# Kernel tuning notes

Measured on AMD Instinct MI355X. Metric: run time of the kernel, lower is better.

Reference implementation:

```python
import jax, jax.numpy as jnp
import numpy as np

B, S, D, V = 4, 512, 512, 32000
GAMMA = 0.5
EPS = 1e-12  # torch F.normalize clamp_min eps


def _l2norm(x, axis):
    n = jnp.sqrt(jnp.sum(x * x, axis=axis, keepdims=True))
    return x / jnp.maximum(n, EPS)


def setup_inputs() -> dict:
    key = jax.random.key(0)
    k1, k2, k3 = jax.random.split(key, 3)
    preds = jax.random.normal(k1, (B, D, S), dtype=jnp.float32)
    emb_weight = jax.random.normal(k2, (V, D), dtype=jnp.float32)
    target = jax.random.randint(k3, (B, S), 0, V, dtype=jnp.int64)
    return {"preds": preds, "emb_weight": emb_weight, "target": target, "pad_id": 0}


def reference(preds, emb_weight, target, pad_id):
    # preds: [B, D, S] -> [B, S, D], L2-normalized over D
    out_norm = _l2norm(jnp.transpose(preds, (0, 2, 1)), axis=2)
    voc_norm = _l2norm(emb_weight, axis=1)          # [V, D]
    tgt_emb = emb_weight[target]                     # [B, S, D] (raw lookup, not normalized)
    mask = target != pad_id                          # [B, S]

    cos_out_voc = jnp.einsum('bsd,vd->bsv', out_norm, voc_norm)  # [B, S, V]
    tgt_voc = jnp.einsum('bsd,vd->bsv', tgt_emb, voc_norm)       # [B, S, V]

    jmax = jnp.argmax(cos_out_voc - tgt_voc, axis=2)             # [B, S]
    cos_target = jnp.take_along_axis(cos_out_voc, target[..., None], axis=2)[..., 0]
    max_cos_voc = jnp.take_along_axis(cos_out_voc, jmax[..., None], axis=2)[..., 0]

    diff = jnp.maximum(GAMMA + max_cos_voc - cos_target, 0.0)    # [B, S]
    denom = jnp.sum(mask).astype(diff.dtype)
    return jnp.sum(jnp.where(mask, diff, 0.0)) / denom
```

## Files before the change

kernel.cpp:

```cpp
#include <hip/hip_runtime.h>
#include <math.h>


#define Bb 4
#define Ss 512
#define Dd 512
#define Vv 32000
#define ROWS (Bb * Ss)
#define NTILE_M (ROWS / 128)
#define NTILE_N (Vv / 128)

typedef __attribute__((ext_vector_type(8))) short bf16x8;
typedef __attribute__((ext_vector_type(4))) float f32x4;

__device__ __forceinline__ float waveReduceSum(float x) {
#pragma unroll
  for (int m = 32; m >= 1; m >>= 1) x += __shfl_xor(x, m, 64);
  return x;
}

__device__ __forceinline__ unsigned short f2bf(float f) {
  unsigned u = __float_as_uint(f);
  unsigned r = (u + 0x7FFFu + ((u >> 16) & 1u)) >> 16;
  return (unsigned short)r;
}

__device__ __forceinline__ unsigned long long packSC(float s, int c) {
  unsigned b = __float_as_uint(s);
  unsigned key = b ^ ((b & 0x80000000u) ? 0xFFFFFFFFu : 0x80000000u);
  return ((unsigned long long)key << 32) | (unsigned)(~c);
}

__device__ __forceinline__ void async_ld16(const void* g, void* l) {
  __builtin_amdgcn_global_load_lds((const __attribute__((address_space(1))) void*)g,
                                   (__attribute__((address_space(3))) void*)l, 16, 0, 0);
}

__global__ __launch_bounds__(256) void prep_rows(
    const float* __restrict__ preds, const float* __restrict__ emb,
    const int* __restrict__ target,
    float* __restrict__ o_rows, short* __restrict__ u_bf,
    float* __restrict__ cos_tgt) {
  int row = blockIdx.x;
  int b = row >> 9, s = row & (Ss - 1);
  int tid = threadIdx.x;
  int wave = tid >> 6, lane = tid & 63;
  const float* p = preds + (size_t)b * Dd * Ss + s;
  float x0 = p[(size_t)tid * Ss];
  float x1 = p[(size_t)(tid + 256) * Ss];
  __shared__ float red[12];
  float ss = waveReduceSum(x0 * x0 + x1 * x1);
  if (lane == 0) red[wave] = ss;
  __syncthreads();
  float inv = 1.0f / fmaxf(sqrtf(red[0] + red[1] + red[2] + red[3]), 1e-12f);
  float o0 = x0 * inv, o1 = x1 * inv;
  o_rows[(size_t)row * Dd + tid] = o0;
  o_rows[(size_t)row * Dd + tid + 256] = o1;
  int t = target[row];
  const float* et = emb + (size_t)t * Dd;
  float e0 = et[tid], e1 = et[tid + 256];
  u_bf[(size_t)row * Dd + tid] = (short)f2bf(o0 - e0);
  u_bf[(size_t)row * Dd + tid + 256] = (short)f2bf(o1 - e1);
  float ss2 = waveReduceSum(e0 * e0 + e1 * e1);
  float dt = waveReduceSum(o0 * e0 + o1 * e1);
  if (lane == 0) { red[4 + wave] = ss2; red[8 + wave] = dt; }
  __syncthreads();
  if (tid == 0) {
    float n2 = red[4] + red[5] + red[6] + red[7];
    float dd = red[8] + red[9] + red[10] + red[11];
    cos_tgt[row] = dd * (1.0f / fmaxf(sqrtf(n2), 1e-12f));
  }
}

__global__ __launch_bounds__(256) void voc_prep(const float* __restrict__ emb,
                                                short* __restrict__ ebf,
                                                float* __restrict__ inv_norm) {
  int v = blockIdx.x * 4 + (threadIdx.x >> 6);
  int lane = threadIdx.x & 63;
  const float* e = emb + (size_t)v * Dd;
  float4 x0 = *(const float4*)(e + lane * 8);
  float4 x1 = *(const float4*)(e + lane * 8 + 4);
  float ss = x0.x * x0.x + x0.y * x0.y + x0.z * x0.z + x0.w * x0.w +
             x1.x * x1.x + x1.y * x1.y + x1.z * x1.z + x1.w * x1.w;
  ss = waveReduceSum(ss);
  float inv = 1.0f / fmaxf(sqrtf(ss), 1e-12f);
  bf16x8 o;
  o[0] = (short)f2bf(x0.x * inv); o[1] = (short)f2bf(x0.y * inv);
  o[2] = (short)f2bf(x0.z * inv); o[3] = (short)f2bf(x0.w * inv);
  o[4] = (short)f2bf(x1.x * inv); o[5] = (short)f2bf(x1.y * inv);
  o[6] = (short)f2bf(x1.z * inv); o[7] = (short)f2bf(x1.w * inv);
  *(bf16x8*)(ebf + (size_t)v * Dd + lane * 8) = o;
  if (lane == 0) inv_norm[v] = inv;
}

__global__ __launch_bounds__(256) void gemm_argmax(
    const short* __restrict__ u_bf, const short* __restrict__ ebf,
    unsigned long long* __restrict__ part) {
  __shared__ short sA[128 * 32];
  __shared__ short sB[128 * 32];
  int tm = blockIdx.x, tn = blockIdx.y;
  int tid = threadIdx.x;
  int w = tid >> 6, lane = tid & 63;
  int wm = w >> 1, wn = w & 1;

  const short* gA = u_bf + ((size_t)(tm * 128 + w * 32 + (lane >> 2)) * Dd) + (lane & 3) * 8;
  const short* gB = ebf + ((size_t)(tn * 128 + w * 32 + (lane >> 2)) * Dd) + (lane & 3) * 8;
  short* lA = &sA[(w * 32) * 32];
  short* lB = &sB[(w * 32) * 32];

  const short* pa = &sA[(lane & 15) * 32 + (lane >> 4) * 8];
  const short* pb = &sB[(lane & 15) * 32 + (lane >> 4) * 8];

  f32x4 acc[4][4];
  f32x4 z = {0.f, 0.f, 0.f, 0.f};
#pragma unroll
  for (int mi = 0; mi < 4; ++mi)
#pragma unroll
    for (int ni = 0; ni < 4; ++ni) acc[mi][ni] = z;

  for (int kk = 0; kk < Dd / 32; ++kk) {
    __syncthreads();
    async_ld16(gA + kk * 32, lA);
    async_ld16(gA + 16 * Dd + kk * 32, lA + 16 * 32);
    async_ld16(gB + kk * 32, lB);
    async_ld16(gB + 16 * Dd + kk * 32, lB + 16 * 32);
    __syncthreads();
    bf16x8 af[4], bg[4];
#pragma unroll
    for (int mi = 0; mi < 4; ++mi)
      af[mi] = *(const bf16x8*)(pa + (wm * 64 + mi * 16) * 32);
#pragma unroll
    for (int ni = 0; ni < 4; ++ni)
      bg[ni] = *(const bf16x8*)(pb + (wn * 64 + ni * 16) * 32);
#pragma unroll
    for (int mi = 0; mi < 4; ++mi)
#pragma unroll
      for (int ni = 0; ni < 4; ++ni)
        acc[mi][ni] = __builtin_amdgcn_mfma_f32_16x16x32_bf16(af[mi], bg[ni], acc[mi][ni], 0, 0, 0);
  }

  float bs[4][4];
  int bc[4][4];
  int col0 = tn * 128 + wn * 64 + (lane & 15);
#pragma unroll
  for (int mi = 0; mi < 4; ++mi) {
#pragma unroll
    for (int j = 0; j < 4; ++j) { bs[mi][j] = acc[mi][0][j]; bc[mi][j] = col0; }
#pragma unroll
    for (int ni = 1; ni < 4; ++ni) {
      int c = col0 + ni * 16;
#pragma unroll
      for (int j = 0; j < 4; ++j) {
        float v = acc[mi][ni][j];
        if (v > bs[mi][j]) { bs[mi][j] = v; bc[mi][j] = c; }
      }
    }
  }
#pragma unroll
  for (int m = 1; m < 16; m <<= 1) {
#pragma unroll
    for (int mi = 0; mi < 4; ++mi)
#pragma unroll
      for (int j = 0; j < 4; ++j) {
        float os = __shfl_xor(bs[mi][j], m, 64);
        int oc = __shfl_xor(bc[mi][j], m, 64);
        if (os > bs[mi][j] || (os == bs[mi][j] && oc < bc[mi][j])) {
          bs[mi][j] = os;
          bc[mi][j] = oc;
        }
      }
  }
  __syncthreads();
  float* sEs = (float*)sA;
  int* sEc = (int*)sA + 256;
  if ((lane & 15) == 0) {
    int q = lane >> 4;
#pragma unroll
    for (int mi = 0; mi < 4; ++mi)
#pragma unroll
      for (int j = 0; j < 4; ++j) {
        int rloc = wm * 64 + mi * 16 + q * 4 + j;
        sEs[wn * 128 + rloc] = bs[mi][j];
        sEc[wn * 128 + rloc] = bc[mi][j];
      }
  }
  __syncthreads();
  if (tid < 128) {
    float s0 = sEs[tid], s1 = sEs[128 + tid];
    int c0 = sEc[tid], c1 = sEc[128 + tid];
    if (s1 > s0 || (s1 == s0 && c1 < c0)) { s0 = s1; c0 = c1; }
    part[(size_t)tn * ROWS + tm * 128 + tid] = packSC(s0, c0);
  }
}

__global__ __launch_bounds__(256) void row_final(
    const float* __restrict__ o_rows, const float* __restrict__ emb,
    const float* __restrict__ inv_norm, const float* __restrict__ cos_tgt,
    const int* __restrict__ target, const int* __restrict__ pad_id,
    const unsigned long long* __restrict__ part, float* __restrict__ diffs) {
  int wave = threadIdx.x >> 6, lane = threadIdx.x & 63;
  int row = blockIdx.x * 4 + wave;
  unsigned long long best = 0ull;
  for (int t = lane; t < NTILE_N; t += 64) {
    unsigned long long p = part[(size_t)t * ROWS + row];
    if (p > best) best = p;
  }
#pragma unroll
  for (int m = 1; m < 64; m <<= 1) {
    unsigned long long o = __shfl_xor(best, m, 64);
    if (o > best) best = o;
  }
  int bi = (int)(~(unsigned)(best & 0xFFFFFFFFull));
  const float* o = o_rows + (size_t)row * Dd;
  const float* e = emb + (size_t)bi * Dd;
  float d = 0.f;
#pragma unroll
  for (int i = 0; i < Dd / 64; ++i) d += o[lane + 64 * i] * e[lane + 64 * i];
  d = waveReduceSum(d);
  if (lane == 0) {
    float cmax = d * inv_norm[bi];
    int t = target[row];
    float df = fmaxf(0.5f + cmax - cos_tgt[row], 0.0f);
    diffs[row] = (t != pad_id[0]) ? df : 0.0f;
  }
}

__global__ __launch_bounds__(256) void reduce_final(
    const float* __restrict__ diffs, const int* __restrict__ target,
    const int* __restrict__ pad_id, float* __restrict__ out) {
  int tid = threadIdx.x;
  int pid = pad_id[0];
  float s = 0.f, c = 0.f;
  for (int i = tid; i < ROWS; i += 256) {
    s += diffs[i];
    c += (target[i] != pid) ? 1.0f : 0.0f;
  }
  s = waveReduceSum(s);
  c = waveReduceSum(c);
  __shared__ float rs[4], rc[4];
  int wave = tid >> 6, lane = tid & 63;
  if (lane == 0) { rs[wave] = s; rc[wave] = c; }
  __syncthreads();
  if (tid == 0) out[0] = (rs[0] + rs[1] + rs[2] + rs[3]) / (rc[0] + rc[1] + rc[2] + rc[3]);
}

extern "C" void kernel_launch(void* const* d_in, const int* in_sizes, int n_in,
                              void* d_out, int out_size, void* d_ws, size_t ws_size,
                              hipStream_t stream) {
  const float* preds = (const float*)d_in[0];
  const float* emb = (const float*)d_in[1];
  const int* target = (const int*)d_in[2];
  const int* pad_id = (const int*)d_in[3];
  char* ws = (char*)d_ws;
  float* o_rows = (float*)ws;
  short* u_bf = (short*)(ws + 4194304);
  short* ebf = (short*)(ws + 6291456);
  float* inv_norm = (float*)(ws + 39059456);
  float* cos_tgt = (float*)(ws + 39187456);
  unsigned long long* part = (unsigned long long*)(ws + 39195648);
  float* diffs = (float*)(ws + 43291648);

  prep_rows<<<ROWS, 256, 0, stream>>>(preds, emb, target, o_rows, u_bf, cos_tgt);
  voc_prep<<<Vv / 4, 256, 0, stream>>>(emb, ebf, inv_norm);
  dim3 g(NTILE_M, NTILE_N);
  gemm_argmax<<<g, 256, 0, stream>>>(u_bf, ebf, part);
  row_final<<<ROWS / 4, 256, 0, stream>>>(o_rows, emb, inv_norm, cos_tgt, target,
                                          pad_id, part, diffs);
  reduce_final<<<1, 256, 0, stream>>>(diffs, target, pad_id, (float*)d_out);
}
```

Baseline: 230.2 us.

## Double-buffer swizzled GEMM tiles and fuse prep and final reduction kernels

The GEMM main loop now double-buffers its LDS tiles. The next K-slice is loaded asynchronously while the current one is consumed, which removes one barrier per iteration. An XOR swizzle on the LDS chunk index is added to cut bank conflicts on fragment reads. The row and vocabulary prep kernels are merged into one launch, and the last reduce kernel is folded into row_final using atomics plus a last-block counter, which removes two launches. The trade-offs are twice the LDS per block and a reliance on float atomics for the final count.

```diff
diff --git a/kernel.cpp b/kernel.cpp
--- a/kernel.cpp
+++ b/kernel.cpp
@@ -9,6 +9,7 @@
 #define ROWS (Bb * Ss)
 #define NTILE_M (ROWS / 128)
 #define NTILE_N (Vv / 128)
+#define VOC_BLOCKS (Vv / 4)
 
 typedef __attribute__((ext_vector_type(8))) short bf16x8;
 typedef __attribute__((ext_vector_type(4))) float f32x4;
@@ -36,80 +37,80 @@
                                    (__attribute__((address_space(3))) void*)l, 16, 0, 0);
 }
 
-__global__ __launch_bounds__(256) void prep_rows(
+__global__ __launch_bounds__(256) void prep_all(
     const float* __restrict__ preds, const float* __restrict__ emb,
     const int* __restrict__ target,
     float* __restrict__ o_rows, short* __restrict__ u_bf,
-    float* __restrict__ cos_tgt) {
-  int row = blockIdx.x;
-  int b = row >> 9, s = row & (Ss - 1);
+    float* __restrict__ cos_tgt, short* __restrict__ ebf,
+    float* __restrict__ inv_norm, float* __restrict__ accum) {
   int tid = threadIdx.x;
   int wave = tid >> 6, lane = tid & 63;
-  const float* p = preds + (size_t)b * Dd * Ss + s;
-  float x0 = p[(size_t)tid * Ss];
-  float x1 = p[(size_t)(tid + 256) * Ss];
-  __shared__ float red[12];
-  float ss = waveReduceSum(x0 * x0 + x1 * x1);
-  if (lane == 0) red[wave] = ss;
-  __syncthreads();
-  float inv = 1.0f / fmaxf(sqrtf(red[0] + red[1] + red[2] + red[3]), 1e-12f);
-  float o0 = x0 * inv, o1 = x1 * inv;
-  o_rows[(size_t)row * Dd + tid] = o0;
-  o_rows[(size_t)row * Dd + tid + 256] = o1;
-  int t = target[row];
-  const float* et = emb + (size_t)t * Dd;
-  float e0 = et[tid], e1 = et[tid + 256];
-  u_bf[(size_t)row * Dd + tid] = (short)f2bf(o0 - e0);
-  u_bf[(size_t)row * Dd + tid + 256] = (short)f2bf(o1 - e1);
-  float ss2 = waveReduceSum(e0 * e0 + e1 * e1);
-  float dt = waveReduceSum(o0 * e0 + o1 * e1);
-  if (lane == 0) { red[4 + wave] = ss2; red[8 + wave] = dt; }
-  __syncthreads();
-  if (tid == 0) {
-    float n2 = red[4] + red[5] + red[6] + red[7];
-    float dd = red[8] + red[9] + red[10] + red[11];
-    cos_tgt[row] = dd * (1.0f / fmaxf(sqrtf(n2), 1e-12f));
-  }
-}
-
-__global__ __launch_bounds__(256) void voc_prep(const float* __restrict__ emb,
-                                                short* __restrict__ ebf,
-                                                float* __restrict__ inv_norm) {
-  int v = blockIdx.x * 4 + (threadIdx.x >> 6);
-  int lane = threadIdx.x & 63;
-  const float* e = emb + (size_t)v * Dd;
-  float4 x0 = *(const float4*)(e + lane * 8);
-  float4 x1 = *(const float4*)(e + lane * 8 + 4);
-  float ss = x0.x * x0.x + x0.y * x0.y + x0.z * x0.z + x0.w * x0.w +
-             x1.x * x1.x + x1.y * x1.y + x1.z * x1.z + x1.w * x1.w;
-  ss = waveReduceSum(ss);
-  float inv = 1.0f / fmaxf(sqrtf(ss), 1e-12f);
-  bf16x8 o;
-  o[0] = (short)f2bf(x0.x * inv); o[1] = (short)f2bf(x0.y * inv);
-  o[2] = (short)f2bf(x0.z * inv); o[3] = (short)f2bf(x0.w * inv);
-  o[4] = (short)f2bf(x1.x * inv); o[5] = (short)f2bf(x1.y * inv);
-  o[6] = (short)f2bf(x1.z * inv); o[7] = (short)f2bf(x1.w * inv);
-  *(bf16x8*)(ebf + (size_t)v * Dd + lane * 8) = o;
-  if (lane == 0) inv_norm[v] = inv;
+  if (blockIdx.x < VOC_BLOCKS) {
+    if (blockIdx.x == 0 && tid < 3) accum[tid] = 0.0f;
+    int v = blockIdx.x * 4 + wave;
+    const float* e = emb + (size_t)v * Dd;
+    float4 x0 = *(const float4*)(e + lane * 8);
+    float4 x1 = *(const float4*)(e + lane * 8 + 4);
+    float ss = x0.x * x0.x + x0.y * x0.y + x0.z * x0.z + x0.w * x0.w +
+               x1.x * x1.x + x1.y * x1.y + x1.z * x1.z + x1.w * x1.w;
+    ss = waveReduceSum(ss);
+    float inv = 1.0f / fmaxf(sqrtf(ss), 1e-12f);
+    bf16x8 o;
+    o[0] = (short)f2bf(x0.x * inv); o[1] = (short)f2bf(x0.y * inv);
+    o[2] = (short)f2bf(x0.z * inv); o[3] = (short)f2bf(x0.w * inv);
+    o[4] = (short)f2bf(x1.x * inv); o[5] = (short)f2bf(x1.y * inv);
+    o[6] = (short)f2bf(x1.z * inv); o[7] = (short)f2bf(x1.w * inv);
+    *(bf16x8*)(ebf + (size_t)v * Dd + lane * 8) = o;
+    if (lane == 0) inv_norm[v] = inv;
+  } else {
+    int row = blockIdx.x - VOC_BLOCKS;
+    int b = row >> 9, s = row & (Ss - 1);
+    const float* p = preds + (size_t)b * Dd * Ss + s;
+    float x0 = p[(size_t)tid * Ss];
+    float x1 = p[(size_t)(tid + 256) * Ss];
+    __shared__ float red[12];
+    float ss = waveReduceSum(x0 * x0 + x1 * x1);
+    if (lane == 0) red[wave] = ss;
+    __syncthreads();
+    float inv = 1.0f / fmaxf(sqrtf(red[0] + red[1] + red[2] + red[3]), 1e-12f);
+    float o0 = x0 * inv, o1 = x1 * inv;
+    o_rows[(size_t)row * Dd + tid] = o0;
+    o_rows[(size_t)row * Dd + tid + 256] = o1;
+    int t = target[row];
+    const float* et = emb + (size_t)t * Dd;
+    float e0 = et[tid], e1 = et[tid + 256];
+    u_bf[(size_t)row * Dd + tid] = (short)f2bf(o0 - e0);
+    u_bf[(size_t)row * Dd + tid + 256] = (short)f2bf(o1 - e1);
+    float ss2 = waveReduceSum(e0 * e0 + e1 * e1);
+    float dt = waveReduceSum(o0 * e0 + o1 * e1);
+    if (lane == 0) { red[4 + wave] = ss2; red[8 + wave] = dt; }
+    __syncthreads();
+    if (tid == 0) {
+      float n2 = red[4] + red[5] + red[6] + red[7];
+      float dd = red[8] + red[9] + red[10] + red[11];
+      cos_tgt[row] = dd * (1.0f / fmaxf(sqrtf(n2), 1e-12f));
+    }
+  }
 }
 
 __global__ __launch_bounds__(256) void gemm_argmax(
     const short* __restrict__ u_bf, const short* __restrict__ ebf,
     unsigned long long* __restrict__ part) {
-  __shared__ short sA[128 * 32];
-  __shared__ short sB[128 * 32];
+  __shared__ short sA[2][128 * 32];
+  __shared__ short sB[2][128 * 32];
   int tm = blockIdx.x, tn = blockIdx.y;
   int tid = threadIdx.x;
   int w = tid >> 6, lane = tid & 63;
   int wm = w >> 1, wn = w & 1;
 
-  const short* gA = u_bf + ((size_t)(tm * 128 + w * 32 + (lane >> 2)) * Dd) + (lane & 3) * 8;
-  const short* gB = ebf + ((size_t)(tn * 128 + w * 32 + (lane >> 2)) * Dd) + (lane & 3) * 8;
-  short* lA = &sA[(w * 32) * 32];
-  short* lB = &sB[(w * 32) * 32];
-
-  const short* pa = &sA[(lane & 15) * 32 + (lane >> 4) * 8];
-  const short* pb = &sB[(lane & 15) * 32 + (lane >> 4) * 8];
+  int srow = w * 32 + (lane >> 2);
+  int schunk = (lane & 3) ^ ((lane >> 4) & 3);
+  const short* gA = u_bf + (size_t)(tm * 128 + srow) * Dd + schunk * 8;
+  const short* gB = ebf + (size_t)(tn * 128 + srow) * Dd + schunk * 8;
+
+  int fr = lane & 15;
+  int pchunk = (lane >> 4) ^ ((fr >> 2) & 3);
+  int foff = fr * 32 + pchunk * 8;
 
   f32x4 acc[4][4];
   f32x4 z = {0.f, 0.f, 0.f, 0.f};
@@ -118,13 +119,30 @@
 #pragma unroll
     for (int ni = 0; ni < 4; ++ni) acc[mi][ni] = z;
 
+  {
+    short* lA = &sA[0][w * 32 * 32];
+    short* lB = &sB[0][w * 32 * 32];
+    async_ld16(gA, lA);
+    async_ld16(gA + 16 * Dd, lA + 16 * 32);
+    async_ld16(gB, lB);
+    async_ld16(gB + 16 * Dd, lB + 16 * 32);
+  }
   for (int kk = 0; kk < Dd / 32; ++kk) {
     __syncthreads();
-    async_ld16(gA + kk * 32, lA);
-    async_ld16(gA + 16 * Dd + kk * 32, lA + 16 * 32);
-    async_ld16(gB + kk * 32, lB);
-    async_ld16(gB + 16 * Dd + kk * 32, lB + 16 * 32);
-    __syncthreads();
+    if (kk < Dd / 32 - 1) {
+      int nb = (kk + 1) & 1;
+      short* lA = &sA[nb][w * 32 * 32];
+      short* lB = &sB[nb][w * 32 * 32];
+      const short* ga = gA + (kk + 1) * 32;
+      const short* gb = gB + (kk + 1) * 32;
+      async_ld16(ga, lA);
+      async_ld16(ga + 16 * Dd, lA + 16 * 32);
+      async_ld16(gb, lB);
+      async_ld16(gb + 16 * Dd, lB + 16 * 32);
+    }
+    int cb = kk & 1;
+    const short* pa = &sA[cb][foff];
+    const short* pb = &sB[cb][foff];
     bf16x8 af[4], bg[4];
 #pragma unroll
     for (int mi = 0; mi < 4; ++mi)
@@ -171,8 +189,8 @@
       }
   }
   __syncthreads();
-  float* sEs = (float*)sA;
-  int* sEc = (int*)sA + 256;
+  float* sEs = (float*)&sA[0][0];
+  int* sEc = (int*)&sA[0][0] + 256;
   if ((lane & 15) == 0) {
     int q = lane >> 4;
 #pragma unroll
@@ -193,11 +211,12 @@
   }
 }
 
-__global__ __launch_bounds__(256) void row_final(
+__global__ __launch_bounds__(256) void row_final_reduce(
     const float* __restrict__ o_rows, const float* __restrict__ emb,
     const float* __restrict__ inv_norm, const float* __restrict__ cos_tgt,
     const int* __restrict__ target, const int* __restrict__ pad_id,
-    const unsigned long long* __restrict__ part, float* __restrict__ diffs) {
+    const unsigned long long* __restrict__ part, float* __restrict__ accum,
+    float* __restrict__ out) {
   int wave = threadIdx.x >> 6, lane = threadIdx.x & 63;
   int row = blockIdx.x * 4 + wave;
   unsigned long long best = 0ull;
@@ -217,31 +236,27 @@
 #pragma unroll
   for (int i = 0; i < Dd / 64; ++i) d += o[lane + 64 * i] * e[lane + 64 * i];
   d = waveReduceSum(d);
+  __shared__ float sdf[4], scn[4];
   if (lane == 0) {
     float cmax = d * inv_norm[bi];
     int t = target[row];
     float df = fmaxf(0.5f + cmax - cos_tgt[row], 0.0f);
-    diffs[row] = (t != pad_id[0]) ? df : 0.0f;
-  }
-}
-
-__global__ __launch_bounds__(256) void reduce_final(
-    const float* __restrict__ diffs, const int* __restrict__ target,
-    const int* __restrict__ pad_id, float* __restrict__ out) {
-  int tid = threadIdx.x;
-  int pid = pad_id[0];
-  float s = 0.f, c = 0.f;
-  for (int i = tid; i < ROWS; i += 256) {
-    s += diffs[i];
-    c += (target[i] != pid) ? 1.0f : 0.0f;
-  }
-  s = waveReduceSum(s);
-  c = waveReduceSum(c);
-  __shared__ float rs[4], rc[4];
-  int wave = tid >> 6, lane = tid & 63;
-  if (lane == 0) { rs[wave] = s; rc[wave] = c; }
+    bool ok = (t != pad_id[0]);
+    sdf[wave] = ok ? df : 0.0f;
+    scn[wave] = ok ? 1.0f : 0.0f;
+  }
   __syncthreads();
-  if (tid == 0) out[0] = (rs[0] + rs[1] + rs[2] + rs[3]) / (rc[0] + rc[1] + rc[2] + rc[3]);
+  if (threadIdx.x == 0) {
+    atomicAdd(&accum[0], sdf[0] + sdf[1] + sdf[2] + sdf[3]);
+    atomicAdd(&accum[1], scn[0] + scn[1] + scn[2] + scn[3]);
+    __threadfence();
+    unsigned t = (unsigned)atomicAdd(&accum[2], 1.0f);
+    if (t == (unsigned)(ROWS / 4 - 1)) {
+      __threadfence();
+      volatile float* va = accum;
+      out[0] = va[0] / va[1];
+    }
+  }
 }
 
 extern "C" void kernel_launch(void* const* d_in, const int* in_sizes, int n_in,
@@ -258,13 +273,13 @@
   float* inv_norm = (float*)(ws + 39059456);
   float* cos_tgt = (float*)(ws + 39187456);
   unsigned long long* part = (unsigned long long*)(ws + 39195648);
-  float* diffs = (float*)(ws + 43291648);
-
-  prep_rows<<<ROWS, 256, 0, stream>>>(preds, emb, target, o_rows, u_bf, cos_tgt);
-  voc_prep<<<Vv / 4, 256, 0, stream>>>(emb, ebf, inv_norm);
+  float* accum = (float*)(ws + 43291648);
+
+  prep_all<<<VOC_BLOCKS + ROWS, 256, 0, stream>>>(preds, emb, target, o_rows, u_bf,
+                                                  cos_tgt, ebf, inv_norm, accum);
   dim3 g(NTILE_M, NTILE_N);
   gemm_argmax<<<g, 256, 0, stream>>>(u_bf, ebf, part);
-  row_final<<<ROWS / 4, 256, 0, stream>>>(o_rows, emb, inv_norm, cos_tgt, target,
-                                          pad_id, part, diffs);
-  reduce_final<<<1, 256, 0, stream>>>(diffs, target, pad_id, (float*)d_out);
-}
+  row_final_reduce<<<ROWS / 4, 256, 0, stream>>>(o_rows, emb, inv_norm, cos_tgt,
+                                                 target, pad_id, part, accum,
+                                                 (float*)d_out);
+}
```

Result: slower. 252.3 us (+9.6%).
